# Performance work log

Measured on AMD Instinct MI355X. Metric: run time of the kernel, lower is better.

Reference implementation:

```python
import jax, jax.numpy as jnp
import numpy as np

B, I, D = 4096, 512, 2048
MAX_DIM = 2560
LEAK_RATE = 0.2
SPIKE_THRESHOLD = 0.5


def setup_inputs() -> dict:
    key = jax.random.key(0)
    k1, k2, k3, k4, k5 = jax.random.split(key, 5)
    return {
        "inputs": jax.random.normal(k1, (B, I), dtype=jnp.float32),
        "state": jax.random.normal(k2, (B, MAX_DIM), dtype=jnp.float32),
        "W_in": jax.random.normal(k3, (D, I), dtype=jnp.float32) * 0.05,
        "W_res": jax.random.normal(k4, (D, D), dtype=jnp.float32) * 0.02,
        "W_gate": jax.random.normal(k5, (3 * D, I), dtype=jnp.float32) * 0.05,
    }


def reference(inputs, state, W_in, W_res, W_gate):
    # Slice previous state to the active reservoir dimension D.
    prev_state = state[:, :D]                                   # [B, D]
    input_part = inputs @ W_in.T                                 # [B, D]
    reservoir_part = prev_state @ W_res.T                        # [B, D]
    gate_part = jax.nn.sigmoid(inputs @ W_gate.T)                # [B, 3D]
    i_gate, f_gate, o_gate = jnp.split(gate_part, 3, axis=-1)
    new_state = (1.0 - LEAK_RATE) * (f_gate * prev_state) \
        + LEAK_RATE * jnp.tanh(i_gate * (input_part + reservoir_part))
    new_state = o_gate * new_state
    # Spike thresholding: subtract threshold where state exceeds it.
    new_state = jnp.where(new_state > SPIKE_THRESHOLD,
                          new_state - SPIKE_THRESHOLD, new_state)
    # Zero-pad active reservoir back to max_dynamic_reservoir_dim.
    padded = jnp.pad(new_state, ((0, 0), (0, MAX_DIM - D)))      # [B, MAX_DIM]
    return padded
```

## Files before the change

### kernel.cpp

```cpp
#include <hip/hip_runtime.h>
#include <math.h>


#define IDIM 512
#define DDIM 2048
#define MAXD 2560
#define BDIM 4096
#define LIST_CAP 262144
#define BAND 4e-3f

typedef __attribute__((ext_vector_type(4))) float f32x4;
typedef __attribute__((ext_vector_type(8))) _Float16 f16x8;

__device__ __forceinline__ void gld16(const unsigned short* g, unsigned short* l) {
    __builtin_amdgcn_global_load_lds((const __attribute__((address_space(1))) void*)g,
                                     (__attribute__((address_space(3))) void*)l,
                                     16, 0, 0);
}
__device__ __forceinline__ float sigf(float x) { return 1.0f / (1.0f + __expf(-x)); }

__global__ __launch_bounds__(256) void convert_kernel(
    const float* __restrict__ x, const float* __restrict__ state,
    const float* __restrict__ win, const float* __restrict__ wgate,
    const float* __restrict__ wres,
    unsigned short* __restrict__ X16, unsigned short* __restrict__ S16,
    unsigned short* __restrict__ Wc16, unsigned short* __restrict__ Wr16,
    float* __restrict__ out, unsigned* __restrict__ cnt)
{
    int idx = blockIdx.x * 256 + threadIdx.x;
    if (idx == 0) *cnt = 0u;
    float4 v;
    unsigned short* p;
    long off;
    if (idx < 524288) {
        v = ((const float4*)x)[idx];
        p = X16; off = (long)idx * 4;
    } else if (idx < 2621440) {
        int i = idx - 524288;
        int row = i >> 9, c4 = i & 511;
        v = *(const float4*)(state + (long)row * MAXD + c4 * 4);
        p = S16; off = (long)i * 4;
    } else if (idx < 3670016) {
        int i = idx - 2621440;
        v = (i < 262144) ? ((const float4*)win)[i] : ((const float4*)wgate)[i - 262144];
        p = Wc16; off = (long)i * 4;
    } else if (idx < 4718592) {
        int i = idx - 3670016;
        v = ((const float4*)wres)[i];
        p = Wr16; off = (long)i * 4;
    } else {
        int i = idx - 4718592;
        int row = i >> 7, c4 = i & 127;
        *(float4*)(out + (long)row * MAXD + DDIM + c4 * 4) = make_float4(0.f, 0.f, 0.f, 0.f);
        return;
    }
    _Float16 h0 = (_Float16)v.x, h1 = (_Float16)v.y;
    _Float16 h2 = (_Float16)v.z, h3 = (_Float16)v.w;
    ushort4 hv;
    hv.x = *(unsigned short*)&h0; hv.y = *(unsigned short*)&h1;
    hv.z = *(unsigned short*)&h2; hv.w = *(unsigned short*)&h3;
    *(ushort4*)(p + off) = hv;
}

__global__ __launch_bounds__(512, 4) void fused_step(
    const unsigned short* __restrict__ X16, const unsigned short* __restrict__ S16,
    const unsigned short* __restrict__ Wc16, const unsigned short* __restrict__ Wr16,
    const float* __restrict__ state, float* __restrict__ out,
    unsigned* __restrict__ cnt, unsigned* __restrict__ list)
{
    __shared__ alignas(16) unsigned short lA[128 * 32];
    __shared__ alignas(16) unsigned short lB[128 * 32];
    const int t = threadIdx.x;
    const int wave = t >> 6, lane = t & 63;
    const int wm = wave >> 2, wn = wave & 3;
    const int quad = lane >> 4, l16 = lane & 15;

    const int bid = blockIdx.x;
    const int nb  = (bid & 7) * 64 + (bid >> 3);
    const int xcd = nb >> 6, lid = nb & 63;
    const int m0 = (((xcd >> 1) << 3) + (lid >> 3)) * 128;
    const int n0 = (((xcd & 1) << 3) + (lid & 7)) * 128;

    const int rowoff = lane >> 2;
    const int kg = ((lane & 3) ^ ((lane >> 3) & 3)) * 8;
    const int krh = (quad ^ ((l16 >> 1) & 3)) * 8;

    f32x4 acc[4][2];
    f32x4 u[4][2];

    #pragma unroll
    for (int mi = 0; mi < 4; mi++)
        #pragma unroll
        for (int ni = 0; ni < 2; ni++)
            acc[mi][ni] = (f32x4)0.0f;

    auto phase = [&](const unsigned short* Ag, long ldA,
                     const unsigned short* Bg, long ldB, int klen) {
        const unsigned short* a0 = Ag + (long)(wave * 16 + rowoff) * ldA + kg;
        const unsigned short* b0 = Bg + (long)(wave * 16 + rowoff) * ldB + kg;
        unsigned short* dA = lA + wave * 512;
        unsigned short* dB = lB + wave * 512;
        for (int k0 = 0; k0 < klen; k0 += 32) {
            __syncthreads();
            gld16(a0 + k0, dA);
            gld16(b0 + k0, dB);
            __syncthreads();
            f16x8 af[4], bf[2];
            #pragma unroll
            for (int mi = 0; mi < 4; mi++)
                af[mi] = *(const f16x8*)&lA[(wm * 64 + mi * 16 + l16) * 32 + krh];
            #pragma unroll
            for (int ni = 0; ni < 2; ni++)
                bf[ni] = *(const f16x8*)&lB[(wn * 32 + ni * 16 + l16) * 32 + krh];
            #pragma unroll
            for (int mi = 0; mi < 4; mi++)
                #pragma unroll
                for (int ni = 0; ni < 2; ni++)
                    acc[mi][ni] = __builtin_amdgcn_mfma_f32_16x16x32_f16(af[mi], bf[ni], acc[mi][ni], 0, 0, 0);
        }
    };

    phase(S16 + (long)m0 * DDIM, DDIM, Wr16 + (long)n0 * DDIM, DDIM, DDIM);
    phase(X16 + (long)m0 * IDIM, IDIM, Wc16 + (long)n0 * IDIM, IDIM, IDIM);
    #pragma unroll
    for (int mi = 0; mi < 4; mi++)
        #pragma unroll
        for (int ni = 0; ni < 2; ni++) { u[mi][ni] = acc[mi][ni]; acc[mi][ni] = (f32x4)0.0f; }

    phase(X16 + (long)m0 * IDIM, IDIM, Wc16 + (long)(DDIM + n0) * IDIM, IDIM, IDIM);
    #pragma unroll
    for (int mi = 0; mi < 4; mi++)
        #pragma unroll
        for (int ni = 0; ni < 2; ni++) {
            #pragma unroll
            for (int r = 0; r < 4; r++)
                u[mi][ni][r] = 0.2f * tanhf(sigf(acc[mi][ni][r]) * u[mi][ni][r]);
            acc[mi][ni] = (f32x4)0.0f;
        }

    phase(X16 + (long)m0 * IDIM, IDIM, Wc16 + (long)(2 * DDIM + n0) * IDIM, IDIM, IDIM);
    #pragma unroll
    for (int mi = 0; mi < 4; mi++)
        #pragma unroll
        for (int ni = 0; ni < 2; ni++) {
            #pragma unroll
            for (int r = 0; r < 4; r++) {
                int row = m0 + wm * 64 + mi * 16 + quad * 4 + r;
                int col = n0 + wn * 32 + ni * 16 + l16;
                float prev = state[(long)row * MAXD + col];
                u[mi][ni][r] += 0.8f * sigf(acc[mi][ni][r]) * prev;
            }
            acc[mi][ni] = (f32x4)0.0f;
        }

    phase(X16 + (long)m0 * IDIM, IDIM, Wc16 + (long)(3 * DDIM + n0) * IDIM, IDIM, IDIM);
    #pragma unroll
    for (int mi = 0; mi < 4; mi++)
        #pragma unroll
        for (int ni = 0; ni < 2; ni++) {
            #pragma unroll
            for (int r = 0; r < 4; r++) {
                int row = m0 + wm * 64 + mi * 16 + quad * 4 + r;
                int col = n0 + wn * 32 + ni * 16 + l16;
                float go = sigf(acc[mi][ni][r]);
                float ns = go * u[mi][ni][r];
                float ov = (ns > 0.5f) ? ns - 0.5f : ns;
                out[(long)row * MAXD + col] = ov;
                if (fabsf(ns - 0.5f) < BAND) {
                    unsigned pos = atomicAdd(cnt, 1u);
                    if (pos < LIST_CAP) list[pos] = (unsigned)(row * DDIM + col);
                }
            }
        }
}

__global__ __launch_bounds__(256) void fixup_kernel(
    const float* __restrict__ x, const float* __restrict__ state,
    const float* __restrict__ win, const float* __restrict__ wres,
    const float* __restrict__ wgate,
    const unsigned* __restrict__ cnt, const unsigned* __restrict__ list,
    float* __restrict__ out)
{
    const int grp  = (blockIdx.x * 256 + threadIdx.x) >> 4;
    const int l16  = threadIdx.x & 15;
    const int ngrp = gridDim.x * 16;
    unsigned n = *cnt;
    if (n > LIST_CAP) n = LIST_CAP;
    for (unsigned e = grp; e < n; e += ngrp) {
        unsigned rc = list[e];
        int row = rc >> 11, col = rc & 2047;
        double ip = 0.0, gi = 0.0, gf = 0.0, go = 0.0, rp = 0.0;
        const float* xr  = x + (long)row * IDIM;
        const float* wi  = win + (long)col * IDIM;
        const float* wgi = wgate + (long)col * IDIM;
        const float* wgf = wgate + (long)(DDIM + col) * IDIM;
        const float* wgo = wgate + (long)(2 * DDIM + col) * IDIM;
        #pragma unroll 2
        for (int k = l16 * 4; k < IDIM; k += 64) {
            float4 xv = *(const float4*)(xr + k);
            float4 a = *(const float4*)(wi + k);
            float4 b = *(const float4*)(wgi + k);
            float4 c = *(const float4*)(wgf + k);
            float4 d = *(const float4*)(wgo + k);
            ip += (double)xv.x * a.x + (double)xv.y * a.y + (double)xv.z * a.z + (double)xv.w * a.w;
            gi += (double)xv.x * b.x + (double)xv.y * b.y + (double)xv.z * b.z + (double)xv.w * b.w;
            gf += (double)xv.x * c.x + (double)xv.y * c.y + (double)xv.z * c.z + (double)xv.w * c.w;
            go += (double)xv.x * d.x + (double)xv.y * d.y + (double)xv.z * d.z + (double)xv.w * d.w;
        }
        const float* sr = state + (long)row * MAXD;
        const float* wr_ = wres + (long)col * DDIM;
        #pragma unroll 4
        for (int k = l16 * 4; k < DDIM; k += 64) {
            float4 sv = *(const float4*)(sr + k);
            float4 wv = *(const float4*)(wr_ + k);
            rp += (double)sv.x * wv.x + (double)sv.y * wv.y + (double)sv.z * wv.z + (double)sv.w * wv.w;
        }
        #pragma unroll
        for (int o = 8; o > 0; o >>= 1) {
            ip += __shfl_down(ip, o, 16);
            gi += __shfl_down(gi, o, 16);
            gf += __shfl_down(gf, o, 16);
            go += __shfl_down(go, o, 16);
            rp += __shfl_down(rp, o, 16);
        }
        if (l16 == 0) {
            double si = 1.0 / (1.0 + exp(-gi));
            double sf = 1.0 / (1.0 + exp(-gf));
            double so = 1.0 / (1.0 + exp(-go));
            double prev = (double)state[(long)row * MAXD + col];
            double ns = so * (0.8 * sf * prev + 0.2 * tanh(si * (ip + rp)));
            if (ns > 0.5) ns -= 0.5;
            out[(long)row * MAXD + col] = (float)ns;
        }
    }
}

extern "C" void kernel_launch(void* const* d_in, const int* in_sizes, int n_in,
                              void* d_out, int out_size, void* d_ws, size_t ws_size,
                              hipStream_t stream) {
    const float* x     = (const float*)d_in[0];
    const float* state = (const float*)d_in[1];
    const float* win   = (const float*)d_in[2];
    const float* wres  = (const float*)d_in[3];
    const float* wgate = (const float*)d_in[4];
    float* out = (float*)d_out;

    char* ws = (char*)d_ws;
    unsigned short* X16  = (unsigned short*)(ws);
    unsigned short* S16  = (unsigned short*)(ws + (4ll  << 20));
    unsigned short* Wc16 = (unsigned short*)(ws + (20ll << 20));
    unsigned short* Wr16 = (unsigned short*)(ws + (28ll << 20));
    unsigned* cnt  = (unsigned*)(ws + (36ll << 20));
    unsigned* list = (unsigned*)(ws + (36ll << 20) + 16);

    convert_kernel<<<dim3(20480), dim3(256), 0, stream>>>(
        x, state, win, wgate, wres, X16, S16, Wc16, Wr16, out, cnt);

    fused_step<<<dim3(512), dim3(512), 0, stream>>>(
        X16, S16, Wc16, Wr16, state, out, cnt, list);

    fixup_kernel<<<dim3(1024), dim3(256), 0, stream>>>(
        x, state, win, wres, wgate, cnt, list, out);
}
```

Before: 377.3 us.

## Bucket fixup entries by column to reuse weight rows in shared memory

Replaces the single global fixup list with per-column buckets (capacity 96 each) plus an overflow list. The fixup kernel now runs one block per column, loads that column's weight rows into LDS once, and has each wave recompute bucketed rows in fp64 from shared weights, with overflow entries handled by a global wave-stride loop. This cuts repeated global weight traffic in the fixup, but adds per-column atomics and a larger 2048-block launch in which most blocks may have little work.

```diff
diff --git a/kernel.cpp b/kernel.cpp
--- a/kernel.cpp
+++ b/kernel.cpp
@@ -6,7 +6,8 @@
 #define DDIM 2048
 #define MAXD 2560
 #define BDIM 4096
-#define LIST_CAP 262144
+#define BCAP 96
+#define OCAP 262144
 #define BAND 4e-3f
 
 typedef __attribute__((ext_vector_type(4))) float f32x4;
@@ -25,10 +26,10 @@
     const float* __restrict__ wres,
     unsigned short* __restrict__ X16, unsigned short* __restrict__ S16,
     unsigned short* __restrict__ Wc16, unsigned short* __restrict__ Wr16,
-    float* __restrict__ out, unsigned* __restrict__ cnt)
+    float* __restrict__ out, unsigned* __restrict__ cntA)
 {
     int idx = blockIdx.x * 256 + threadIdx.x;
-    if (idx == 0) *cnt = 0u;
+    if (idx < 2052) cntA[idx] = 0u;
     float4 v;
     unsigned short* p;
     long off;
@@ -66,7 +67,7 @@
     const unsigned short* __restrict__ X16, const unsigned short* __restrict__ S16,
     const unsigned short* __restrict__ Wc16, const unsigned short* __restrict__ Wr16,
     const float* __restrict__ state, float* __restrict__ out,
-    unsigned* __restrict__ cnt, unsigned* __restrict__ list)
+    unsigned* __restrict__ cntA, unsigned* __restrict__ bl, unsigned* __restrict__ ol)
 {
     __shared__ alignas(16) unsigned short lA[128 * 32];
     __shared__ alignas(16) unsigned short lB[128 * 32];
@@ -153,6 +154,9 @@
             acc[mi][ni] = (f32x4)0.0f;
         }
 
+    #pragma unroll
+    for (int mi = 0; mi < 4; mi++)
+        (void)0;
     phase(X16 + (long)m0 * IDIM, IDIM, Wc16 + (long)(3 * DDIM + n0) * IDIM, IDIM, IDIM);
     #pragma unroll
     for (int mi = 0; mi < 4; mi++)
@@ -167,8 +171,13 @@
                 float ov = (ns > 0.5f) ? ns - 0.5f : ns;
                 out[(long)row * MAXD + col] = ov;
                 if (fabsf(ns - 0.5f) < BAND) {
-                    unsigned pos = atomicAdd(cnt, 1u);
-                    if (pos < LIST_CAP) list[pos] = (unsigned)(row * DDIM + col);
+                    unsigned pos = atomicAdd(&cntA[col], 1u);
+                    if (pos < BCAP) {
+                        bl[col * BCAP + pos] = (unsigned)row;
+                    } else {
+                        unsigned op = atomicAdd(&cntA[2048], 1u);
+                        if (op < OCAP) ol[op] = (unsigned)((row << 11) | col);
+                    }
                 }
             }
         }
@@ -178,52 +187,108 @@
     const float* __restrict__ x, const float* __restrict__ state,
     const float* __restrict__ win, const float* __restrict__ wres,
     const float* __restrict__ wgate,
-    const unsigned* __restrict__ cnt, const unsigned* __restrict__ list,
-    float* __restrict__ out)
+    const unsigned* __restrict__ cntA, const unsigned* __restrict__ bl,
+    const unsigned* __restrict__ ol, float* __restrict__ out)
 {
-    const int grp  = (blockIdx.x * 256 + threadIdx.x) >> 4;
-    const int l16  = threadIdx.x & 15;
-    const int ngrp = gridDim.x * 16;
-    unsigned n = *cnt;
-    if (n > LIST_CAP) n = LIST_CAP;
-    for (unsigned e = grp; e < n; e += ngrp) {
-        unsigned rc = list[e];
-        int row = rc >> 11, col = rc & 2047;
+    __shared__ float sWin[512], sWi[512], sWf[512], sWo[512];
+    __shared__ float sWr[2048];
+    const int c = blockIdx.x;
+    const int t = threadIdx.x;
+    const int wave = t >> 6, lane = t & 63;
+
+    unsigned m = cntA[c]; if (m > BCAP) m = BCAP;
+    if (m > 0) {
+        for (int k = t; k < 512; k += 256) {
+            sWin[k] = win[(long)c * IDIM + k];
+            sWi[k]  = wgate[(long)c * IDIM + k];
+            sWf[k]  = wgate[(long)(DDIM + c) * IDIM + k];
+            sWo[k]  = wgate[(long)(2 * DDIM + c) * IDIM + k];
+        }
+        for (int k = t; k < 2048; k += 256)
+            sWr[k] = wres[(long)c * DDIM + k];
+        __syncthreads();
+
+        for (unsigned e = wave; e < m; e += 4) {
+            int row = (int)bl[c * BCAP + e];
+            double ip = 0.0, gi = 0.0, gf = 0.0, go = 0.0, rp = 0.0;
+            const float* xr = x + (long)row * IDIM;
+            #pragma unroll 2
+            for (int k = lane * 4; k < IDIM; k += 256) {
+                float4 xv = *(const float4*)(xr + k);
+                ip += (double)xv.x * (double)sWin[k]   + (double)xv.y * (double)sWin[k+1]
+                    + (double)xv.z * (double)sWin[k+2] + (double)xv.w * (double)sWin[k+3];
+                gi += (double)xv.x * (double)sWi[k]    + (double)xv.y * (double)sWi[k+1]
+                    + (double)xv.z * (double)sWi[k+2]  + (double)xv.w * (double)sWi[k+3];
+                gf += (double)xv.x * (double)sWf[k]    + (double)xv.y * (double)sWf[k+1]
+                    + (double)xv.z * (double)sWf[k+2]  + (double)xv.w * (double)sWf[k+3];
+                go += (double)xv.x * (double)sWo[k]    + (double)xv.y * (double)sWo[k+1]
+                    + (double)xv.z * (double)sWo[k+2]  + (double)xv.w * (double)sWo[k+3];
+            }
+            const float* sr = state + (long)row * MAXD;
+            #pragma unroll 4
+            for (int k = lane * 4; k < DDIM; k += 256) {
+                float4 sv = *(const float4*)(sr + k);
+                rp += (double)sv.x * (double)sWr[k]   + (double)sv.y * (double)sWr[k+1]
+                    + (double)sv.z * (double)sWr[k+2] + (double)sv.w * (double)sWr[k+3];
+            }
+            #pragma unroll
+            for (int o = 32; o > 0; o >>= 1) {
+                ip += __shfl_down(ip, o);
+                gi += __shfl_down(gi, o);
+                gf += __shfl_down(gf, o);
+                go += __shfl_down(go, o);
+                rp += __shfl_down(rp, o);
+            }
+            if (lane == 0) {
+                double si = 1.0 / (1.0 + exp(-gi));
+                double sf = 1.0 / (1.0 + exp(-gf));
+                double so = 1.0 / (1.0 + exp(-go));
+                double prev = (double)state[(long)row * MAXD + c];
+                double ns = so * (0.8 * sf * prev + 0.2 * tanh(si * (ip + rp)));
+                if (ns > 0.5) ns -= 0.5;
+                out[(long)row * MAXD + c] = (float)ns;
+            }
+        }
+    }
+
+    unsigned nof = cntA[2048]; if (nof > OCAP) nof = OCAP;
+    const int gw = blockIdx.x * 4 + wave;
+    for (unsigned e = gw; e < nof; e += 2048 * 4) {
+        unsigned rc = ol[e];
+        int row = (int)(rc >> 11), col = (int)(rc & 2047);
         double ip = 0.0, gi = 0.0, gf = 0.0, go = 0.0, rp = 0.0;
         const float* xr  = x + (long)row * IDIM;
         const float* wi  = win + (long)col * IDIM;
         const float* wgi = wgate + (long)col * IDIM;
         const float* wgf = wgate + (long)(DDIM + col) * IDIM;
         const float* wgo = wgate + (long)(2 * DDIM + col) * IDIM;
-        #pragma unroll 2
-        for (int k = l16 * 4; k < IDIM; k += 64) {
+        for (int k = lane * 4; k < IDIM; k += 256) {
             float4 xv = *(const float4*)(xr + k);
             float4 a = *(const float4*)(wi + k);
             float4 b = *(const float4*)(wgi + k);
-            float4 c = *(const float4*)(wgf + k);
+            float4 cc = *(const float4*)(wgf + k);
             float4 d = *(const float4*)(wgo + k);
             ip += (double)xv.x * a.x + (double)xv.y * a.y + (double)xv.z * a.z + (double)xv.w * a.w;
             gi += (double)xv.x * b.x + (double)xv.y * b.y + (double)xv.z * b.z + (double)xv.w * b.w;
-            gf += (double)xv.x * c.x + (double)xv.y * c.y + (double)xv.z * c.z + (double)xv.w * c.w;
+            gf += (double)xv.x * cc.x + (double)xv.y * cc.y + (double)xv.z * cc.z + (double)xv.w * cc.w;
             go += (double)xv.x * d.x + (double)xv.y * d.y + (double)xv.z * d.z + (double)xv.w * d.w;
         }
         const float* sr = state + (long)row * MAXD;
         const float* wr_ = wres + (long)col * DDIM;
-        #pragma unroll 4
-        for (int k = l16 * 4; k < DDIM; k += 64) {
+        for (int k = lane * 4; k < DDIM; k += 256) {
             float4 sv = *(const float4*)(sr + k);
             float4 wv = *(const float4*)(wr_ + k);
             rp += (double)sv.x * wv.x + (double)sv.y * wv.y + (double)sv.z * wv.z + (double)sv.w * wv.w;
         }
         #pragma unroll
-        for (int o = 8; o > 0; o >>= 1) {
-            ip += __shfl_down(ip, o, 16);
-            gi += __shfl_down(gi, o, 16);
-            gf += __shfl_down(gf, o, 16);
-            go += __shfl_down(go, o, 16);
-            rp += __shfl_down(rp, o, 16);
-        }
-        if (l16 == 0) {
+        for (int o = 32; o > 0; o >>= 1) {
+            ip += __shfl_down(ip, o);
+            gi += __shfl_down(gi, o);
+            gf += __shfl_down(gf, o);
+            go += __shfl_down(go, o);
+            rp += __shfl_down(rp, o);
+        }
+        if (lane == 0) {
             double si = 1.0 / (1.0 + exp(-gi));
             double sf = 1.0 / (1.0 + exp(-gf));
             double so = 1.0 / (1.0 + exp(-go));
@@ -250,15 +315,16 @@
     unsigned short* S16  = (unsigned short*)(ws + (4ll  << 20));
     unsigned short* Wc16 = (unsigned short*)(ws + (20ll << 20));
     unsigned short* Wr16 = (unsigned short*)(ws + (28ll << 20));
-    unsigned* cnt  = (unsigned*)(ws + (36ll << 20));
-    unsigned* list = (unsigned*)(ws + (36ll << 20) + 16);
+    unsigned* cntA = (unsigned*)(ws + (36ll << 20));
+    unsigned* bl   = (unsigned*)(ws + (36ll << 20) + (16ll << 10));
+    unsigned* ol   = (unsigned*)(ws + (37ll << 20));
 
     convert_kernel<<<dim3(20480), dim3(256), 0, stream>>>(
-        x, state, win, wgate, wres, X16, S16, Wc16, Wr16, out, cnt);
+        x, state, win, wgate, wres, X16, S16, Wc16, Wr16, out, cntA);
 
     fused_step<<<dim3(512), dim3(512), 0, stream>>>(
-        X16, S16, Wc16, Wr16, state, out, cnt, list);
-
-    fixup_kernel<<<dim3(1024), dim3(256), 0, stream>>>(
-        x, state, win, wres, wgate, cnt, list, out);
-}
+        X16, S16, Wc16, Wr16, state, out, cntA, bl, ol);
+
+    fixup_kernel<<<dim3(2048), dim3(256), 0, stream>>>(
+        x, state, win, wres, wgate, cntA, bl, ol, out);
+}
```

New measurement: 336.4 us. 1.12x faster.
